# Performance work log

Hardware: AMD Instinct MI355X
Metric: run time of the kernel (lower is better)

Reference implementation:

```python
import jax, jax.numpy as jnp
import numpy as np

N, D, C = 2048, 192, 100000
S, M = 30.0, 0.2

def setup_inputs() -> dict:
    key = jax.random.key(0)
    k1, k2, k3 = jax.random.split(key, 3)
    x = jax.random.normal(k1, (N, D), dtype=jnp.float32)
    W = jax.random.normal(k2, (C, D), dtype=jnp.float32) * 0.05
    label = jax.random.randint(k3, (N,), 0, C, dtype=jnp.int64)
    return {"x": x, "W": W, "label": label}

def reference(x, W, label):
    # NOTE: the original torch code's weight-normalization loop is a no-op
    # (it rebinds the local name W, never mutating the parameter), so W is
    # intentionally NOT normalized here; only x is.
    xn = x / jnp.linalg.norm(x, axis=1, keepdims=True)          # [N, D]
    wf = jnp.einsum("nd,cd->nc", xn, W)                          # [N, C]
    tgt = jnp.take_along_axis(wf, label[:, None], axis=1)[:, 0]  # [N]
    numer = S * (tgt - M)                                        # margin-adjusted target logit
    logits = S * wf
    # replace the label column with the margin-adjusted numerator so that
    # logsumexp(logits) == log(exp(numer) + sum_{j!=y} exp(s*wf[:,j]))
    logits = logits.at[jnp.arange(N), label].set(numer)
    L = numer - jax.nn.logsumexp(logits, axis=1)                 # [N]
    return -jnp.mean(L)
```

## Files before the change

### kernel.cpp

```cpp
#include <hip/hip_runtime.h>
#include <stdint.h>


constexpr int N  = 2048;
constexpr int D  = 192;
constexpr int C  = 100000;
constexpr int KT = D / 32;
constexpr int TILE = 512;
constexpr int RT16 = C / 16;
constexpr int TPG = 12;
constexpr int CX = 523;
constexpr int NT16 = CX * TPG;
constexpr float PHANTOM = (float)(NT16 * 16 - C);
constexpr int BANDS = 4;
constexpr int RYB = N / (64 * BANDS);
constexpr int BUF = 4 * KT * TILE;
constexpr int NXB = N / 4;
constexpr int CXP = 528;

#define S_SCALE 30.0f
#define MARGIN  0.2f
#define S_LOG2E 43.2808512266689f

using short8 = __attribute__((ext_vector_type(8))) short;
using f32x4  = __attribute__((ext_vector_type(4))) float;

typedef __attribute__((address_space(1))) const void GV;
typedef __attribute__((address_space(3))) void LV;

__device__ inline unsigned short f2bf(float f) {
  unsigned int u = __float_as_uint(f);
  u += 0x7fffu + ((u >> 16) & 1u);
  return (unsigned short)(u >> 16);
}

__device__ inline unsigned int cvtpk(float lo, float hi) {
  unsigned int r;
  asm("v_cvt_pk_bf16_f32 %0, %1, %2" : "=v"(r) : "v"(lo), "v"(hi));
  return r;
}

__device__ inline int pack_idx(int r, int k) {
  return ((r >> 4) * KT + (k >> 5)) * TILE + (((k >> 3) & 3) * 16 + (r & 15)) * 8 + (k & 7);
}

__device__ inline float row_sum16(float v) {
  int x;
  x = __float_as_int(v);
  v += __int_as_float(__builtin_amdgcn_update_dpp(0, x, 0x128, 0xF, 0xF, true));
  x = __float_as_int(v);
  v += __int_as_float(__builtin_amdgcn_update_dpp(0, x, 0x124, 0xF, 0xF, true));
  x = __float_as_int(v);
  v += __int_as_float(__builtin_amdgcn_update_dpp(0, x, 0x04E, 0xF, 0xF, true));
  x = __float_as_int(v);
  v += __int_as_float(__builtin_amdgcn_update_dpp(0, x, 0x0B1, 0xF, 0xF, true));
  return v;
}

__global__ __launch_bounds__(256) void prep_all(
    const float* __restrict__ x, const float* __restrict__ W,
    const int* __restrict__ label,
    unsigned short* __restrict__ xnb, unsigned short* __restrict__ Wb,
    float* __restrict__ aux, float* __restrict__ rowsum,
    float* __restrict__ out) {
  const int bid  = blockIdx.x;
  const int lane = threadIdx.x & 63;
  if (bid == 0 && threadIdx.x == 0) out[0] = 0.0f;

  if (bid < NXB) {
    const int row = bid * 4 + (threadIdx.x >> 6);
    const float* xr = x + (size_t)row * D;
    float v0 = xr[lane], v1 = xr[lane + 64], v2 = xr[lane + 128];
    float ss = v0 * v0 + v1 * v1 + v2 * v2;
    const int lab = label[row];
    const float* wr = W + (size_t)lab * D;
    float d = v0 * wr[lane] + v1 * wr[lane + 64] + v2 * wr[lane + 128];
#pragma unroll
    for (int off = 32; off > 0; off >>= 1) {
      ss += __shfl_xor(ss, off, 64);
      d  += __shfl_xor(d,  off, 64);
    }
    const float rinv = rsqrtf(ss);
    const float inv = rinv * S_LOG2E;
    xnb[pack_idx(row, lane)]       = f2bf(v0 * inv);
    xnb[pack_idx(row, lane + 64)]  = f2bf(v1 * inv);
    xnb[pack_idx(row, lane + 128)] = f2bf(v2 * inv);
    if (lane == 0) {
      aux[row]    = d * rinv;
      rowsum[row] = 0.0f;
    }
  } else {
    const int t16 = (bid - NXB) * 4 + (threadIdx.x >> 6);
    const int m = lane & 15, q = lane >> 4;
    unsigned short* dst = Wb + (size_t)t16 * KT * TILE + lane * 8;
    if (t16 < RT16) {
      const float* src = W + (size_t)(t16 * 16 + m) * D + q * 8;
#pragma unroll
      for (int ks = 0; ks < KT; ++ks) {
        const float4* s4 = (const float4*)(src + ks * 32);
        float4 f0 = s4[0], f1 = s4[1];
        union { uint4 u; short8 s; } cv;
        cv.u.x = cvtpk(f0.x, f0.y);
        cv.u.y = cvtpk(f0.z, f0.w);
        cv.u.z = cvtpk(f1.x, f1.y);
        cv.u.w = cvtpk(f1.z, f1.w);
        *(short8*)(dst + (size_t)ks * TILE) = cv.s;
      }
    } else {
      const short8 z = {0, 0, 0, 0, 0, 0, 0, 0};
#pragma unroll
      for (int ks = 0; ks < KT; ++ks) *(short8*)(dst + (size_t)ks * TILE) = z;
    }
  }
}

__global__ __launch_bounds__(256, 3) void gemm_lse(
    const unsigned short* __restrict__ xnb,
    const unsigned short* __restrict__ Wb,
    float* __restrict__ rowsum) {
  __shared__ alignas(16) unsigned short As[2 * BUF];
  __shared__ alignas(16) float rs_lds[4][256];

  const int tid = threadIdx.x;
  const int bid = blockIdx.x;
  const int xcd = bid & 7, j = bid >> 3;
  const int ry = j & 7;
  const int cx = (j >> 3) * 8 + xcd;
  if (cx >= CX) return;

  {
    const unsigned short* slab = xnb + (size_t)(ry * BANDS) * BUF;
#pragma unroll
    for (int i = 0; i < 6; ++i) {
      const int chunk = tid + i * 256;
      __builtin_amdgcn_global_load_lds(
          (GV*)((const char*)slab + (size_t)chunk * 16),
          (LV*)((char*)As + (size_t)chunk * 16), 16, 0, 0);
    }
  }

  const int lane = tid & 63, wave = tid >> 6;
  const int m = lane & 15, quad = lane >> 4;

  short8 breg[3][KT];
#pragma unroll
  for (int tc = 0; tc < 3; ++tc)
#pragma unroll
    for (int ks = 0; ks < KT; ++ks)
      breg[tc][ks] = *(const short8*)(
          Wb + (size_t)((cx * TPG + wave * 3 + tc) * KT + ks) * TILE + lane * 8);

  const f32x4 zero4 = {0.0f, 0.0f, 0.0f, 0.0f};

  for (int b = 0; b < BANDS; ++b) {
    __syncthreads();

    if (b + 1 < BANDS) {
      const unsigned short* slab = xnb + (size_t)(ry * BANDS + b + 1) * BUF;
      char* dst = (char*)&As[((b + 1) & 1) * BUF];
#pragma unroll
      for (int i = 0; i < 6; ++i) {
        const int chunk = tid + i * 256;
        __builtin_amdgcn_global_load_lds(
            (GV*)((const char*)slab + (size_t)chunk * 16),
            (LV*)(dst + (size_t)chunk * 16), 16, 0, 0);
      }
    }

    const unsigned short* Ab = &As[(b & 1) * BUF];

    f32x4 acc[4][3];
#pragma unroll
    for (int a = 0; a < 4; ++a)
#pragma unroll
      for (int c = 0; c < 3; ++c) acc[a][c] = zero4;

#pragma unroll
    for (int ks = 0; ks < KT; ++ks) {
      short8 af[4];
#pragma unroll
      for (int tr = 0; tr < 4; ++tr)
        af[tr] = *(const short8*)(&Ab[(tr * KT + ks) * TILE + lane * 8]);
#pragma unroll
      for (int tr = 0; tr < 4; ++tr)
#pragma unroll
        for (int tc = 0; tc < 3; ++tc)
          acc[tr][tc] = __builtin_amdgcn_mfma_f32_16x16x32_bf16(
              af[tr], breg[tc][ks], acc[tr][tc], 0, 0, 0);
    }

#pragma unroll
    for (int tr = 0; tr < 4; ++tr) {
      float rv0 = 0.f, rv1 = 0.f, rv2 = 0.f, rv3 = 0.f;
#pragma unroll
      for (int tc = 0; tc < 3; ++tc) {
        rv0 += __builtin_amdgcn_exp2f(acc[tr][tc][0]);
        rv1 += __builtin_amdgcn_exp2f(acc[tr][tc][1]);
        rv2 += __builtin_amdgcn_exp2f(acc[tr][tc][2]);
        rv3 += __builtin_amdgcn_exp2f(acc[tr][tc][3]);
      }
      rv0 = row_sum16(rv0);
      rv1 = row_sum16(rv1);
      rv2 = row_sum16(rv2);
      rv3 = row_sum16(rv3);
      if (m == 0) {
        float4 v = make_float4(rv0, rv1, rv2, rv3);
        *(float4*)(&rs_lds[wave][b * 64 + tr * 16 + quad * 4]) = v;
      }
    }
  }

  __syncthreads();
  const float s = rs_lds[0][tid] + rs_lds[1][tid] + rs_lds[2][tid] + rs_lds[3][tid];
  atomicAdd(&rowsum[ry * 256 + tid], s);
}

__global__ __launch_bounds__(256) void finalize_tiny(
    const float* __restrict__ aux, const float* __restrict__ rowsum,
    float* __restrict__ out) {
  const int row  = blockIdx.x * 256 + threadIdx.x;
  const int lane = threadIdx.x & 63, wave = threadIdx.x >> 6;
  const float tgt   = aux[row];
  const float numer = S_SCALE * (tgt - MARGIN);
  const float se = rowsum[row] - PHANTOM - __expf(S_SCALE * tgt) + __expf(numer);
  float L = numer - logf(se);
#pragma unroll
  for (int off = 32; off > 0; off >>= 1) L += __shfl_xor(L, off, 64);
  __shared__ float part[4];
  if (lane == 0) part[wave] = L;
  __syncthreads();
  if (threadIdx.x == 0) {
    const float blocksum = part[0] + part[1] + part[2] + part[3];
    atomicAdd(out, -blocksum * (1.0f / (float)N));
  }
}

extern "C" void kernel_launch(void* const* d_in, const int* in_sizes, int n_in,
                              void* d_out, int out_size, void* d_ws, size_t ws_size,
                              hipStream_t stream) {
  const float* x     = (const float*)d_in[0];
  const float* W     = (const float*)d_in[1];
  const int*   label = (const int*)d_in[2];
  float*       out   = (float*)d_out;

  char* ws = (char*)d_ws;
  size_t off = 0;
  unsigned short* xnb = (unsigned short*)(ws + off); off += (size_t)N * D * 2;
  unsigned short* Wb  = (unsigned short*)(ws + off); off += (size_t)NT16 * KT * TILE * 2;
  float* aux    = (float*)(ws + off); off += (size_t)N * 4;
  float* rowsum = (float*)(ws + off); off += (size_t)N * 4;

  prep_all<<<NXB + NT16 / 4, 256, 0, stream>>>(x, W, label, xnb, Wb, aux, rowsum, out);

  gemm_lse<<<CXP * RYB, 256, 0, stream>>>(xnb, Wb, rowsum);

  finalize_tiny<<<N / 256, 256, 0, stream>>>(aux, rowsum, out);
}
```

Baseline: 203.9 us.

## Fuse finalize into GEMM via last-block counter and batch W loads in prep

Removes the separate finalize kernel launch: each GEMM block increments a global counter after its rowsum atomics, and the last block computes the per-row loss and writes the mean. The prep kernel also resets the counter and now issues all W float4 loads before converting, to increase memory-level parallelism. This saves one launch and its gap, at the cost of a fence and atomic per block and a serial tail on one block.

```diff
diff --git a/kernel.cpp b/kernel.cpp
--- a/kernel.cpp
+++ b/kernel.cpp
@@ -17,6 +17,7 @@
 constexpr int BUF = 4 * KT * TILE;
 constexpr int NXB = N / 4;
 constexpr int CXP = 528;
+constexpr int REAL_BLOCKS = CX * RYB;
 
 #define S_SCALE 30.0f
 #define MARGIN  0.2f
@@ -62,10 +63,10 @@
     const int* __restrict__ label,
     unsigned short* __restrict__ xnb, unsigned short* __restrict__ Wb,
     float* __restrict__ aux, float* __restrict__ rowsum,
-    float* __restrict__ out) {
+    unsigned int* __restrict__ cnt, float* __restrict__ out) {
   const int bid  = blockIdx.x;
   const int lane = threadIdx.x & 63;
-  if (bid == 0 && threadIdx.x == 0) out[0] = 0.0f;
+  if (bid == 0 && threadIdx.x == 0) { out[0] = 0.0f; *cnt = 0u; }
 
   if (bid < NXB) {
     const int row = bid * 4 + (threadIdx.x >> 6);
@@ -95,15 +96,20 @@
     unsigned short* dst = Wb + (size_t)t16 * KT * TILE + lane * 8;
     if (t16 < RT16) {
       const float* src = W + (size_t)(t16 * 16 + m) * D + q * 8;
+      float4 f[2 * KT];
 #pragma unroll
       for (int ks = 0; ks < KT; ++ks) {
         const float4* s4 = (const float4*)(src + ks * 32);
-        float4 f0 = s4[0], f1 = s4[1];
+        f[2 * ks]     = s4[0];
+        f[2 * ks + 1] = s4[1];
+      }
+#pragma unroll
+      for (int ks = 0; ks < KT; ++ks) {
         union { uint4 u; short8 s; } cv;
-        cv.u.x = cvtpk(f0.x, f0.y);
-        cv.u.y = cvtpk(f0.z, f0.w);
-        cv.u.z = cvtpk(f1.x, f1.y);
-        cv.u.w = cvtpk(f1.z, f1.w);
+        cv.u.x = cvtpk(f[2 * ks].x,     f[2 * ks].y);
+        cv.u.y = cvtpk(f[2 * ks].z,     f[2 * ks].w);
+        cv.u.z = cvtpk(f[2 * ks + 1].x, f[2 * ks + 1].y);
+        cv.u.w = cvtpk(f[2 * ks + 1].z, f[2 * ks + 1].w);
         *(short8*)(dst + (size_t)ks * TILE) = cv.s;
       }
     } else {
@@ -117,9 +123,13 @@
 __global__ __launch_bounds__(256, 3) void gemm_lse(
     const unsigned short* __restrict__ xnb,
     const unsigned short* __restrict__ Wb,
-    float* __restrict__ rowsum) {
+    const float* __restrict__ aux,
+    float* __restrict__ rowsum,
+    unsigned int* __restrict__ cnt,
+    float* __restrict__ out) {
   __shared__ alignas(16) unsigned short As[2 * BUF];
   __shared__ alignas(16) float rs_lds[4][256];
+  __shared__ int last_flag;
 
   const int tid = threadIdx.x;
   const int bid = blockIdx.x;
@@ -213,25 +223,33 @@
   __syncthreads();
   const float s = rs_lds[0][tid] + rs_lds[1][tid] + rs_lds[2][tid] + rs_lds[3][tid];
   atomicAdd(&rowsum[ry * 256 + tid], s);
-}
-
-__global__ __launch_bounds__(256) void finalize_tiny(
-    const float* __restrict__ aux, const float* __restrict__ rowsum,
-    float* __restrict__ out) {
-  const int row  = blockIdx.x * 256 + threadIdx.x;
-  const int lane = threadIdx.x & 63, wave = threadIdx.x >> 6;
-  const float tgt   = aux[row];
-  const float numer = S_SCALE * (tgt - MARGIN);
-  const float se = rowsum[row] - PHANTOM - __expf(S_SCALE * tgt) + __expf(numer);
-  float L = numer - logf(se);
-#pragma unroll
-  for (int off = 32; off > 0; off >>= 1) L += __shfl_xor(L, off, 64);
-  __shared__ float part[4];
-  if (lane == 0) part[wave] = L;
+
+  __threadfence();
   __syncthreads();
-  if (threadIdx.x == 0) {
-    const float blocksum = part[0] + part[1] + part[2] + part[3];
-    atomicAdd(out, -blocksum * (1.0f / (float)N));
+  if (tid == 0) {
+    const unsigned int p = __hip_atomic_fetch_add(
+        cnt, 1u, __ATOMIC_ACQ_REL, __HIP_MEMORY_SCOPE_AGENT);
+    last_flag = (p == (unsigned int)(REAL_BLOCKS - 1));
+  }
+  __syncthreads();
+  if (last_flag) {
+    __threadfence();
+    float L = 0.0f;
+    for (int r = tid; r < N; r += 256) {
+      const float rsv = __hip_atomic_load(&rowsum[r], __ATOMIC_RELAXED,
+                                          __HIP_MEMORY_SCOPE_AGENT);
+      const float tgt   = aux[r];
+      const float numer = S_SCALE * (tgt - MARGIN);
+      const float se = rsv - PHANTOM - __expf(S_SCALE * tgt) + __expf(numer);
+      L += numer - logf(se);
+    }
+#pragma unroll
+    for (int off = 32; off > 0; off >>= 1) L += __shfl_xor(L, off, 64);
+    if (lane == 0) rs_lds[0][wave] = L;
+    __syncthreads();
+    if (tid == 0)
+      out[0] = -(rs_lds[0][0] + rs_lds[0][1] + rs_lds[0][2] + rs_lds[0][3]) *
+               (1.0f / (float)N);
   }
 }
 
@@ -249,10 +267,9 @@
   unsigned short* Wb  = (unsigned short*)(ws + off); off += (size_t)NT16 * KT * TILE * 2;
   float* aux    = (float*)(ws + off); off += (size_t)N * 4;
   float* rowsum = (float*)(ws + off); off += (size_t)N * 4;
-
-  prep_all<<<NXB + NT16 / 4, 256, 0, stream>>>(x, W, label, xnb, Wb, aux, rowsum, out);
-
-  gemm_lse<<<CXP * RYB, 256, 0, stream>>>(xnb, Wb, rowsum);
-
-  finalize_tiny<<<N / 256, 256, 0, stream>>>(aux, rowsum, out);
-}
+  unsigned int* cnt = (unsigned int*)(ws + off); off += 128;
+
+  prep_all<<<NXB + NT16 / 4, 256, 0, stream>>>(x, W, label, xnb, Wb, aux, rowsum, cnt, out);
+
+  gemm_lse<<<CXP * RYB, 256, 0, stream>>>(xnb, Wb, aux, rowsum, cnt, out);
+}
```

Result: slower. 514.6 us (+152.4%).

## Software-pipeline MFMA half-bands with exp2 epilogue and batch W loads in prep

Applied to the files above, without the earlier changes.

The GEMM band loop is split into two half-bands with separate accumulator sets and fully unrolled, so the exp2/row-sum epilogue of one half is interleaved with the MFMAs of the next half. The aim is to overlap transcendental and DPP work with matrix-core work and hide the epilogue latency. In prep, all W float4 loads for a tile are issued before any conversion to increase memory-level parallelism. Register pressure stays at two 2x3 accumulator sets, which may affect occupancy under launch_bounds(256,3).

```diff
diff --git a/kernel.cpp b/kernel.cpp
--- a/kernel.cpp
+++ b/kernel.cpp
@@ -95,15 +95,20 @@
     unsigned short* dst = Wb + (size_t)t16 * KT * TILE + lane * 8;
     if (t16 < RT16) {
       const float* src = W + (size_t)(t16 * 16 + m) * D + q * 8;
+      float4 f[2 * KT];
 #pragma unroll
       for (int ks = 0; ks < KT; ++ks) {
         const float4* s4 = (const float4*)(src + ks * 32);
-        float4 f0 = s4[0], f1 = s4[1];
+        f[2 * ks]     = s4[0];
+        f[2 * ks + 1] = s4[1];
+      }
+#pragma unroll
+      for (int ks = 0; ks < KT; ++ks) {
         union { uint4 u; short8 s; } cv;
-        cv.u.x = cvtpk(f0.x, f0.y);
-        cv.u.y = cvtpk(f0.z, f0.w);
-        cv.u.z = cvtpk(f1.x, f1.y);
-        cv.u.w = cvtpk(f1.z, f1.w);
+        cv.u.x = cvtpk(f[2 * ks].x,     f[2 * ks].y);
+        cv.u.y = cvtpk(f[2 * ks].z,     f[2 * ks].w);
+        cv.u.z = cvtpk(f[2 * ks + 1].x, f[2 * ks + 1].y);
+        cv.u.w = cvtpk(f[2 * ks + 1].z, f[2 * ks + 1].w);
         *(short8*)(dst + (size_t)ks * TILE) = cv.s;
       }
     } else {
@@ -113,6 +118,65 @@
     }
   }
 }
+
+#define PREFETCH(BN)                                                          \
+  {                                                                           \
+    const unsigned short* slab = xnb + (size_t)(ry * BANDS + (BN)) * BUF;     \
+    char* dst = (char*)&As[((BN) & 1) * BUF];                                 \
+    _Pragma("unroll")                                                         \
+    for (int i = 0; i < 6; ++i) {                                             \
+      const int chunk = tid + i * 256;                                        \
+      __builtin_amdgcn_global_load_lds(                                       \
+          (GV*)((const char*)slab + (size_t)chunk * 16),                      \
+          (LV*)(dst + (size_t)chunk * 16), 16, 0, 0);                         \
+    }                                                                         \
+  }
+
+#define KH(BIDX, H, ACC)                                                      \
+  {                                                                           \
+    const unsigned short* Ab = &As[((BIDX) & 1) * BUF];                       \
+    _Pragma("unroll")                                                         \
+    for (int t2 = 0; t2 < 2; ++t2)                                            \
+      _Pragma("unroll")                                                       \
+      for (int c = 0; c < 3; ++c) ACC[t2][c] = zero4;                         \
+    _Pragma("unroll")                                                         \
+    for (int ks = 0; ks < KT; ++ks) {                                         \
+      const short8 af0 =                                                      \
+          *(const short8*)(&Ab[(((H) * 2 + 0) * KT + ks) * TILE + lane * 8]); \
+      const short8 af1 =                                                      \
+          *(const short8*)(&Ab[(((H) * 2 + 1) * KT + ks) * TILE + lane * 8]); \
+      _Pragma("unroll")                                                       \
+      for (int c = 0; c < 3; ++c)                                             \
+        ACC[0][c] = __builtin_amdgcn_mfma_f32_16x16x32_bf16(                  \
+            af0, breg[c][ks], ACC[0][c], 0, 0, 0);                            \
+      _Pragma("unroll")                                                       \
+      for (int c = 0; c < 3; ++c)                                             \
+        ACC[1][c] = __builtin_amdgcn_mfma_f32_16x16x32_bf16(                  \
+            af1, breg[c][ks], ACC[1][c], 0, 0, 0);                            \
+    }                                                                         \
+  }
+
+#define EPI(ACC, BIDX, H)                                                     \
+  {                                                                           \
+    _Pragma("unroll")                                                         \
+    for (int t2 = 0; t2 < 2; ++t2) {                                          \
+      float rv0 = 0.f, rv1 = 0.f, rv2 = 0.f, rv3 = 0.f;                       \
+      _Pragma("unroll")                                                       \
+      for (int c = 0; c < 3; ++c) {                                           \
+        rv0 += __builtin_amdgcn_exp2f(ACC[t2][c][0]);                         \
+        rv1 += __builtin_amdgcn_exp2f(ACC[t2][c][1]);                         \
+        rv2 += __builtin_amdgcn_exp2f(ACC[t2][c][2]);                         \
+        rv3 += __builtin_amdgcn_exp2f(ACC[t2][c][3]);                         \
+      }                                                                       \
+      rv0 = row_sum16(rv0);                                                   \
+      rv1 = row_sum16(rv1);                                                   \
+      rv2 = row_sum16(rv2);                                                   \
+      rv3 = row_sum16(rv3);                                                   \
+      if (m == 0)                                                             \
+        *(float4*)(&rs_lds[wave][(BIDX) * 64 + (H) * 32 + t2 * 16 + quad * 4]) = \
+            make_float4(rv0, rv1, rv2, rv3);                                  \
+    }                                                                         \
+  }
 
 __global__ __launch_bounds__(256, 3) void gemm_lse(
     const unsigned short* __restrict__ xnb,
@@ -151,64 +215,24 @@
           Wb + (size_t)((cx * TPG + wave * 3 + tc) * KT + ks) * TILE + lane * 8);
 
   const f32x4 zero4 = {0.0f, 0.0f, 0.0f, 0.0f};
-
-  for (int b = 0; b < BANDS; ++b) {
-    __syncthreads();
-
-    if (b + 1 < BANDS) {
-      const unsigned short* slab = xnb + (size_t)(ry * BANDS + b + 1) * BUF;
-      char* dst = (char*)&As[((b + 1) & 1) * BUF];
-#pragma unroll
-      for (int i = 0; i < 6; ++i) {
-        const int chunk = tid + i * 256;
-        __builtin_amdgcn_global_load_lds(
-            (GV*)((const char*)slab + (size_t)chunk * 16),
-            (LV*)(dst + (size_t)chunk * 16), 16, 0, 0);
-      }
-    }
-
-    const unsigned short* Ab = &As[(b & 1) * BUF];
-
-    f32x4 acc[4][3];
-#pragma unroll
-    for (int a = 0; a < 4; ++a)
-#pragma unroll
-      for (int c = 0; c < 3; ++c) acc[a][c] = zero4;
-
-#pragma unroll
-    for (int ks = 0; ks < KT; ++ks) {
-      short8 af[4];
-#pragma unroll
-      for (int tr = 0; tr < 4; ++tr)
-        af[tr] = *(const short8*)(&Ab[(tr * KT + ks) * TILE + lane * 8]);
-#pragma unroll
-      for (int tr = 0; tr < 4; ++tr)
-#pragma unroll
-        for (int tc = 0; tc < 3; ++tc)
-          acc[tr][tc] = __builtin_amdgcn_mfma_f32_16x16x32_bf16(
-              af[tr], breg[tc][ks], acc[tr][tc], 0, 0, 0);
-    }
-
-#pragma unroll
-    for (int tr = 0; tr < 4; ++tr) {
-      float rv0 = 0.f, rv1 = 0.f, rv2 = 0.f, rv3 = 0.f;
-#pragma unroll
-      for (int tc = 0; tc < 3; ++tc) {
-        rv0 += __builtin_amdgcn_exp2f(acc[tr][tc][0]);
-        rv1 += __builtin_amdgcn_exp2f(acc[tr][tc][1]);
-        rv2 += __builtin_amdgcn_exp2f(acc[tr][tc][2]);
-        rv3 += __builtin_amdgcn_exp2f(acc[tr][tc][3]);
-      }
-      rv0 = row_sum16(rv0);
-      rv1 = row_sum16(rv1);
-      rv2 = row_sum16(rv2);
-      rv3 = row_sum16(rv3);
-      if (m == 0) {
-        float4 v = make_float4(rv0, rv1, rv2, rv3);
-        *(float4*)(&rs_lds[wave][b * 64 + tr * 16 + quad * 4]) = v;
-      }
-    }
-  }
+  f32x4 accA[2][3], accB[2][3];
+
+  __syncthreads();
+  PREFETCH(1);
+  KH(0, 0, accA);
+  KH(0, 1, accB); EPI(accA, 0, 0);
+  __syncthreads();
+  PREFETCH(2);
+  KH(1, 0, accA); EPI(accB, 0, 1);
+  KH(1, 1, accB); EPI(accA, 1, 0);
+  __syncthreads();
+  PREFETCH(3);
+  KH(2, 0, accA); EPI(accB, 1, 1);
+  KH(2, 1, accB); EPI(accA, 2, 0);
+  __syncthreads();
+  KH(3, 0, accA); EPI(accB, 2, 1);
+  KH(3, 1, accB); EPI(accA, 3, 0);
+  EPI(accB, 3, 1);
 
   __syncthreads();
   const float s = rs_lds[0][tid] + rs_lds[1][tid] + rs_lds[2][tid] + rs_lds[3][tid];
```

Result: no change. 202.3 us (-0.8%).
